# Performance work log

Hardware: AMD Instinct MI355X
Metric: run time of the kernel (lower is better)

## Reference

```python
import jax, jax.numpy as jnp
import numpy as np
from jax import lax

NUM_CHANNELS = 32
PROT_SECTION = 4
PROT_SIZE = NUM_CHANNELS * PROT_SECTION  # 128
BATCH = 128
SEQ_LEN = 8194


def setup_inputs() -> dict:
    key = jax.random.key(0)
    ks = jax.random.split(key, 6)
    input_seq = jax.random.randint(ks[0], (BATCH, SEQ_LEN), 0, 26)
    emb = jax.random.normal(ks[1], (26, 5), dtype=jnp.float32)
    conv_w = jax.random.normal(ks[2], (NUM_CHANNELS, 5, 3), dtype=jnp.float32) * 0.1
    conv_b = jnp.zeros((NUM_CHANNELS,), dtype=jnp.float32)
    W_a = jax.random.normal(ks[3], (PROT_SIZE, PROT_SIZE), dtype=jnp.float32) / np.sqrt(PROT_SIZE)
    v_a = jax.random.normal(ks[4], (PROT_SIZE,), dtype=jnp.float32)
    return {"input_seq": input_seq, "emb": emb, "conv_w": conv_w,
            "conv_b": conv_b, "W_a": W_a, "v_a": v_a}


def reference(input_seq, emb, conv_w, conv_b, W_a, v_a):
    # Embedding lookup: [B, L, 5] -> [B, 5, L]
    x = emb[input_seq].transpose(0, 2, 1)
    # Conv1d(5 -> C, k=3, valid) + bias + ReLU  (dropout is identity in eval)
    y = lax.conv_general_dilated(x, conv_w, window_strides=(1,), padding='VALID',
                                 dimension_numbers=('NCH', 'OIH', 'NCH'))
    y = jax.nn.relu(y + conv_b[None, :, None])  # [B, C, L-2]
    B, C, PL = y.shape
    S = PROT_SECTION
    new_L = PL // S
    rem = PL % S
    head = rem // 2
    tail = PL - (rem - head)
    y = y[:, :, head:tail].reshape(B, C * S, new_L)  # [B, D, N], D = C*S
    # Batched self-attention pooling (original loops over batch in Python)
    # energies[b, n] = v_a @ tanh(W_a @ H_b)
    e = jnp.einsum('d,bdn->bn', v_a, jnp.tanh(jnp.einsum('de,ben->bdn', W_a, y)))
    w = jax.nn.softmax(e, axis=-1)  # stable softmax; same math as unstable F.softmax
    ctx = jnp.einsum('bn,bdn->bd', w, y)  # [B, D]
    return ctx
```

## Files before the change

kernel.cpp:

```cpp
#include <hip/hip_runtime.h>

#define LSEQ 8194

typedef _Float16 f16x8 __attribute__((ext_vector_type(8)));
typedef _Float16 f16x2 __attribute__((ext_vector_type(2)));
typedef __attribute__((ext_vector_type(4))) float f32x4;

static __device__ __forceinline__ float tanh_fast(float x){
    float p = __expf(2.0f * x);
    float r = __builtin_amdgcn_rcpf(1.0f + p);
    return 1.0f - 2.0f * r;
}
static __device__ __forceinline__ unsigned h3relu(unsigned a, unsigned b, unsigned c){
    union { f16x2 h; unsigned u; } x, y, z, r;
    x.u = a; y.u = b; z.u = c;
    f16x2 s = x.h + y.h + z.h;
    f16x2 zero = { (_Float16)0.0f, (_Float16)0.0f };
    r.h = __builtin_elementwise_max(s, zero);
    return r.u;
}
static __device__ __forceinline__ unsigned hpack(float a, float b){
    union { f16x2 h; unsigned u; } pk;
    pk.h = (f16x2){ (_Float16)a, (_Float16)b };
    return pk.u;
}
#define ROR_ADD(x, ctrl) ({ \
    union { float f; int i; } _s, _r; _s.f = (x); \
    _r.i = __builtin_amdgcn_update_dpp(0, _s.i, (ctrl), 0xF, 0xF, true); \
    (x) + _r.f; })

__global__ __launch_bounds__(256) void k_setup(
        const float* __restrict__ emb, const float* __restrict__ cw,
        const float* __restrict__ cb, const float* __restrict__ Wa,
        unsigned* __restrict__ tblG, unsigned* __restrict__ wahG)
{
    int gid = blockIdx.x*256 + threadIdx.x;
    if (gid < 1248){
        int k = gid / 416;
        int rem = gid - k*416;
        int l = rem >> 4;
        int cp = rem & 15;
        int c0 = cp*2;
        float v0 = 0.f, v1 = 0.f;
        #pragma unroll
        for (int i = 0; i < 5; i++){
            float e = emb[l*5 + i];
            v0 += cw[(c0*5 + i)*3 + k] * e;
            v1 += cw[((c0+1)*5 + i)*3 + k] * e;
        }
        if (k == 2){ v0 += cb[c0]; v1 += cb[c0+1]; }
        tblG[k*520 + l*20 + (cp & 3)*4 + (cp >> 2)] = hpack(v0, v1);
    }
    for (int u = gid; u < 2048; u += 1280){
        int lane = u & 63, dtki = u >> 6;
        int dt = dtki >> 2, ki = dtki & 3;
        int m = lane & 15, q = lane >> 4;
        const float2* src = (const float2*)Wa + ((dt*16 + m)*64 + ki*16 + q*4);
        float2 s0 = src[0], s1 = src[1], s2 = src[2], s3 = src[3];
        uint4 o;
        o.x = hpack(s0.x, s0.y);
        o.y = hpack(s1.x, s1.y);
        o.z = hpack(s2.x, s2.y);
        o.w = hpack(s3.x, s3.y);
        ((uint4*)wahG)[u] = o;
    }
}

__global__ __launch_bounds__(256, 2) void k_fused(
        const int* __restrict__ seq, const unsigned* __restrict__ tblG,
        const unsigned* __restrict__ wahG, const float* __restrict__ va,
        float* __restrict__ part, float* __restrict__ stats)
{
    __shared__ __align__(16) unsigned tblH[1560];
    __shared__ unsigned short seqw16[4][132];
    __shared__ __align__(16) float vaL[128];

    int tid = threadIdx.x;
    int b   = blockIdx.y;
    int x   = blockIdx.x;
    int n0  = x * 128;

    for (int i = tid; i < 390; i += 256)
        ((uint4*)tblH)[i] = ((const uint4*)tblG)[i];
    if (tid < 128) vaL[tid] = va[tid];
    const int* sb = seq + (size_t)b * LSEQ;
    for (int i = tid; i < 4*132; i += 256){
        int s = i / 132, off = i - s*132;
        if (off < 130)
            seqw16[s][off] = (unsigned short)(sb[s*2048 + n0 + off] * 80);
    }
    __syncthreads();

    int w = tid >> 6, lane = tid & 63;
    int m = lane & 15, q = lane >> 4;
    const char* tb0 = (const char*)tblH + q*16;
    const char* tb1 = tb0 + 2080;
    const char* tb2 = tb1 + 2080;
    const uint4* wa4 = (const uint4*)wahG + lane;

    uint4 vfr0[4], vfr1[4];
    {
        int base = w*32 + m;
        unsigned V[4][4];
        #pragma unroll
        for (int s = 0; s < 4; s++){
            unsigned oa = seqw16[s][base];
            unsigned ob = seqw16[s][base+1];
            unsigned oc = seqw16[s][base+2];
            uint4 t0 = *(const uint4*)(tb0 + oa);
            uint4 t1 = *(const uint4*)(tb1 + ob);
            uint4 t2 = *(const uint4*)(tb2 + oc);
            V[s][0] = h3relu(t0.x, t1.x, t2.x);
            V[s][1] = h3relu(t0.y, t1.y, t2.y);
            V[s][2] = h3relu(t0.z, t1.z, t2.z);
            V[s][3] = h3relu(t0.w, t1.w, t2.w);
        }
        #pragma unroll
        for (int ki = 0; ki < 4; ki++){
            uint4 o;
            o.x = __builtin_amdgcn_perm(V[1][ki], V[0][ki], 0x05040100u);
            o.y = __builtin_amdgcn_perm(V[3][ki], V[2][ki], 0x05040100u);
            o.z = __builtin_amdgcn_perm(V[1][ki], V[0][ki], 0x07060302u);
            o.w = __builtin_amdgcn_perm(V[3][ki], V[2][ki], 0x07060302u);
            vfr0[ki] = o;
        }
    }
    {
        int base = w*32 + 16 + m;
        unsigned V[4][4];
        #pragma unroll
        for (int s = 0; s < 4; s++){
            unsigned oa = seqw16[s][base];
            unsigned ob = seqw16[s][base+1];
            unsigned oc = seqw16[s][base+2];
            uint4 t0 = *(const uint4*)(tb0 + oa);
            uint4 t1 = *(const uint4*)(tb1 + ob);
            uint4 t2 = *(const uint4*)(tb2 + oc);
            V[s][0] = h3relu(t0.x, t1.x, t2.x);
            V[s][1] = h3relu(t0.y, t1.y, t2.y);
            V[s][2] = h3relu(t0.z, t1.z, t2.z);
            V[s][3] = h3relu(t0.w, t1.w, t2.w);
        }
        #pragma unroll
        for (int ki = 0; ki < 4; ki++){
            uint4 o;
            o.x = __builtin_amdgcn_perm(V[1][ki], V[0][ki], 0x05040100u);
            o.y = __builtin_amdgcn_perm(V[3][ki], V[2][ki], 0x05040100u);
            o.z = __builtin_amdgcn_perm(V[1][ki], V[0][ki], 0x07060302u);
            o.w = __builtin_amdgcn_perm(V[3][ki], V[2][ki], 0x07060302u);
            vfr1[ki] = o;
        }
    }

    float ep0 = 0.f, ep1 = 0.f;
    #pragma unroll
    for (int h = 0; h < 2; h++){
        f32x4 acc0[4], acc1[4];
        #pragma unroll
        for (int dd = 0; dd < 4; dd++){
            acc0[dd] = (f32x4){0.f, 0.f, 0.f, 0.f};
            acc1[dd] = (f32x4){0.f, 0.f, 0.f, 0.f};
        }
        #pragma unroll
        for (int kp = 0; kp < 2; kp++){
            uint4 af[8];
            #pragma unroll
            for (int kk = 0; kk < 2; kk++)
                #pragma unroll
                for (int dd = 0; dd < 4; dd++){
                    int dt = h*4 + dd, ki = kp*2 + kk;
                    af[kk*4+dd] = wa4[(dt*4 + ki) << 6];
                }
            #pragma unroll
            for (int kk = 0; kk < 2; kk++){
                int ki = kp*2 + kk;
                union { uint4 u; f16x8 f; } b0, b1;
                b0.u = vfr0[ki]; b1.u = vfr1[ki];
                #pragma unroll
                for (int dd = 0; dd < 4; dd++){
                    union { uint4 u; f16x8 f; } a; a.u = af[kk*4+dd];
                    acc0[dd] = __builtin_amdgcn_mfma_f32_16x16x32_f16(a.f, b0.f, acc0[dd], 0, 0, 0);
                    acc1[dd] = __builtin_amdgcn_mfma_f32_16x16x32_f16(a.f, b1.f, acc1[dd], 0, 0, 0);
                }
            }
        }
        #pragma unroll
        for (int dd = 0; dd < 4; dd++){
            int dt = h*4 + dd;
            const f32x4 vg = *(const f32x4*)&vaL[dt*16 + q*4];
            ep0 += vg[0] * tanh_fast(acc0[dd][0]);
            ep0 += vg[1] * tanh_fast(acc0[dd][1]);
            ep0 += vg[2] * tanh_fast(acc0[dd][2]);
            ep0 += vg[3] * tanh_fast(acc0[dd][3]);
            ep1 += vg[0] * tanh_fast(acc1[dd][0]);
            ep1 += vg[1] * tanh_fast(acc1[dd][1]);
            ep1 += vg[2] * tanh_fast(acc1[dd][2]);
            ep1 += vg[3] * tanh_fast(acc1[dd][3]);
        }
    }
    ep0 += __shfl_xor(ep0, 16);
    ep0 += __shfl_xor(ep0, 32);
    ep1 += __shfl_xor(ep1, 16);
    ep1 += __shfl_xor(ep1, 32);

    float w0 = __expf(ep0);
    float w1 = __expf(ep1);
    float Sw = w0 + w1;

    float accp[32];
    #pragma unroll
    for (int ki = 0; ki < 4; ki++){
        union { uint4 u; f16x2 h[4]; } v0, v1;
        v0.u = vfr0[ki]; v1.u = vfr1[ki];
        accp[ki*8 + 0] = w0 * (float)v0.h[0][0] + w1 * (float)v1.h[0][0];
        accp[ki*8 + 1] = w0 * (float)v0.h[0][1] + w1 * (float)v1.h[0][1];
        accp[ki*8 + 2] = w0 * (float)v0.h[1][0] + w1 * (float)v1.h[1][0];
        accp[ki*8 + 3] = w0 * (float)v0.h[1][1] + w1 * (float)v1.h[1][1];
        accp[ki*8 + 4] = w0 * (float)v0.h[2][0] + w1 * (float)v1.h[2][0];
        accp[ki*8 + 5] = w0 * (float)v0.h[2][1] + w1 * (float)v1.h[2][1];
        accp[ki*8 + 6] = w0 * (float)v0.h[3][0] + w1 * (float)v1.h[3][0];
        accp[ki*8 + 7] = w0 * (float)v0.h[3][1] + w1 * (float)v1.h[3][1];
    }

    #pragma unroll
    for (int j = 0; j < 32; j++){
        accp[j] = ROR_ADD(accp[j], 0x121);
        accp[j] = ROR_ADD(accp[j], 0x122);
        accp[j] = ROR_ADD(accp[j], 0x124);
        accp[j] = ROR_ADD(accp[j], 0x128);
    }
    Sw = ROR_ADD(Sw, 0x121);
    Sw = ROR_ADD(Sw, 0x122);
    Sw = ROR_ADD(Sw, 0x124);
    Sw = ROR_ADD(Sw, 0x128);

    size_t chunk = ((size_t)b*16 + x)*4 + w;
    if (m == 0){
        float* pd = part + chunk*128;
        #pragma unroll
        for (int ki = 0; ki < 4; ki++){
            float4 lo = { accp[ki*8+0], accp[ki*8+1], accp[ki*8+2], accp[ki*8+3] };
            float4 hi = { accp[ki*8+4], accp[ki*8+5], accp[ki*8+6], accp[ki*8+7] };
            *(float4*)(pd + ki*32 + q*8)     = lo;
            *(float4*)(pd + ki*32 + q*8 + 4) = hi;
        }
    }
    if (lane == 0)
        stats[chunk] = Sw;
}

__global__ __launch_bounds__(128) void kb2_finish(const float* __restrict__ part,
        const float* __restrict__ stats, float* __restrict__ out)
{
    int b = blockIdx.x, d = threadIdx.x;
    const float* st = stats + (size_t)b*64;
    float S = 0.f;
    #pragma unroll 8
    for (int c = 0; c < 64; c++) S += st[c];
    const float* p = part + (size_t)b*64*128 + d;
    float s = 0.f;
    #pragma unroll 8
    for (int c = 0; c < 64; c++) s += p[c*128];
    out[b*128 + d] = s / S;
}

extern "C" void kernel_launch(void* const* d_in, const int* in_sizes, int n_in,
                              void* d_out, int out_size, void* d_ws, size_t ws_size,
                              hipStream_t stream)
{
    const int*   seq = (const int*)d_in[0];
    const float* emb = (const float*)d_in[1];
    const float* cw  = (const float*)d_in[2];
    const float* cb  = (const float*)d_in[3];
    const float* Wa  = (const float*)d_in[4];
    const float* va  = (const float*)d_in[5];
    float* out = (float*)d_out;

    char* wsb = (char*)d_ws;
    float*    part  = (float*)wsb;
    float*    stats = (float*)(wsb + (8<<20));
    unsigned* tblG  = (unsigned*)(wsb + (12<<20));
    unsigned* wahG  = (unsigned*)(wsb + (12<<20) + 32768);

    k_setup   <<<5,            256, 0, stream>>>(emb, cw, cb, Wa, tblG, wahG);
    k_fused   <<<dim3(16,128), 256, 0, stream>>>(seq, tblG, wahG, va, part, stats);
    kb2_finish<<<128,          128, 0, stream>>>(part, stats, out);
}
```

Measured before the change: 93.96 us.

## Pad conv lookup table rows in LDS and fuse DPP row reductions into adds

```diff
diff --git a/kernel.cpp b/kernel.cpp
--- a/kernel.cpp
+++ b/kernel.cpp
@@ -24,10 +24,12 @@
     pk.h = (f16x2){ (_Float16)a, (_Float16)b };
     return pk.u;
 }
-#define ROR_ADD(x, ctrl) ({ \
-    union { float f; int i; } _s, _r; _s.f = (x); \
-    _r.i = __builtin_amdgcn_update_dpp(0, _s.i, (ctrl), 0xF, 0xF, true); \
-    (x) + _r.f; })
+#define ROR_ADD(x, rorstr) ({ \
+    float _r; \
+    asm("s_nop 1\n\t" \
+        "v_add_f32_dpp %0, %1, %1 " rorstr " row_mask:0xf bank_mask:0xf" \
+        : "=v"(_r) : "v"(x)); \
+    _r; })
 
 __global__ __launch_bounds__(256) void k_setup(
         const float* __restrict__ emb, const float* __restrict__ cw,
@@ -49,8 +51,14 @@
             v1 += cw[((c0+1)*5 + i)*3 + k] * e;
         }
         if (k == 2){ v0 += cb[c0]; v1 += cb[c0+1]; }
-        tblG[k*520 + l*20 + (cp & 3)*4 + (cp >> 2)] = hpack(v0, v1);
-    }
+        tblG[k*546 + l*21 + (cp & 3)*4 + (cp >> 2)] = hpack(v0, v1);
+    }
+    if (gid >= 1248 && gid < 1248 + 390){
+        int pg = gid - 1248;
+        int row = pg / 5, pw = pg - row*5;
+        tblG[row*21 + 16 + pw] = 0u;
+    }
+    if (gid < 8) tblG[1638 + gid] = 0u;
     for (int u = gid; u < 2048; u += 1280){
         int lane = u & 63, dtki = u >> 6;
         int dt = dtki >> 2, ki = dtki & 3;
@@ -71,7 +79,7 @@
         const unsigned* __restrict__ wahG, const float* __restrict__ va,
         float* __restrict__ part, float* __restrict__ stats)
 {
-    __shared__ __align__(16) unsigned tblH[1560];
+    __shared__ __align__(16) unsigned tblH[1648];
     __shared__ unsigned short seqw16[4][132];
     __shared__ __align__(16) float vaL[128];
 
@@ -80,22 +88,22 @@
     int x   = blockIdx.x;
     int n0  = x * 128;
 
-    for (int i = tid; i < 390; i += 256)
+    for (int i = tid; i < 412; i += 256)
         ((uint4*)tblH)[i] = ((const uint4*)tblG)[i];
     if (tid < 128) vaL[tid] = va[tid];
     const int* sb = seq + (size_t)b * LSEQ;
     for (int i = tid; i < 4*132; i += 256){
         int s = i / 132, off = i - s*132;
         if (off < 130)
-            seqw16[s][off] = (unsigned short)(sb[s*2048 + n0 + off] * 80);
+            seqw16[s][off] = (unsigned short)(sb[s*2048 + n0 + off] * 84);
     }
     __syncthreads();
 
     int w = tid >> 6, lane = tid & 63;
     int m = lane & 15, q = lane >> 4;
     const char* tb0 = (const char*)tblH + q*16;
-    const char* tb1 = tb0 + 2080;
-    const char* tb2 = tb1 + 2080;
+    const char* tb1 = tb0 + 2184;
+    const char* tb2 = tb1 + 2184;
     const uint4* wa4 = (const uint4*)wahG + lane;
 
     uint4 vfr0[4], vfr1[4];
@@ -224,15 +232,15 @@
 
     #pragma unroll
     for (int j = 0; j < 32; j++){
-        accp[j] = ROR_ADD(accp[j], 0x121);
-        accp[j] = ROR_ADD(accp[j], 0x122);
-        accp[j] = ROR_ADD(accp[j], 0x124);
-        accp[j] = ROR_ADD(accp[j], 0x128);
-    }
-    Sw = ROR_ADD(Sw, 0x121);
-    Sw = ROR_ADD(Sw, 0x122);
-    Sw = ROR_ADD(Sw, 0x124);
-    Sw = ROR_ADD(Sw, 0x128);
+        accp[j] = ROR_ADD(accp[j], "row_ror:1");
+        accp[j] = ROR_ADD(accp[j], "row_ror:2");
+        accp[j] = ROR_ADD(accp[j], "row_ror:4");
+        accp[j] = ROR_ADD(accp[j], "row_ror:8");
+    }
+    Sw = ROR_ADD(Sw, "row_ror:1");
+    Sw = ROR_ADD(Sw, "row_ror:2");
+    Sw = ROR_ADD(Sw, "row_ror:4");
+    Sw = ROR_ADD(Sw, "row_ror:8");
 
     size_t chunk = ((size_t)b*16 + x)*4 + w;
     if (m == 0){
```

Result: slower. 104.1 us (+10.8%).
